# Optimization experiments

Measured on AMD Instinct MI355X. Metric: run time of the kernel, lower is better.

## Reference

```python
import jax, jax.numpy as jnp
import numpy as np

UNITS = 256  # LSTM hidden size per source (units=256)

def setup_inputs() -> dict:
    key = jax.random.key(0)
    ks = jax.random.split(key, 7)
    vocab, embed_dim, seq_len, batch, n_cls = 50000, 256, 512, 64, 20
    x = jax.random.randint(ks[0], (batch, seq_len), 0, vocab)
    emb = jax.random.normal(ks[1], (vocab, embed_dim), jnp.float32) * 0.05
    W = jax.random.normal(ks[2], (embed_dim, 4 * UNITS), jnp.float32) * (1.0 / np.sqrt(embed_dim))
    U = jax.random.normal(ks[3], (UNITS, 4 * UNITS), jnp.float32) * (1.0 / np.sqrt(UNITS))
    # keras unit_forget_bias: forget-gate bias = 1, others 0 (gate order i,f,c,o)
    b = jnp.concatenate([jnp.zeros((UNITS,)), jnp.ones((UNITS,)), jnp.zeros((2 * UNITS,))]).astype(jnp.float32)
    Wd = jax.random.normal(ks[4], (UNITS, n_cls), jnp.float32) * (1.0 / np.sqrt(UNITS))
    bd = jnp.zeros((n_cls,), jnp.float32)
    return {"x": x, "emb": emb, "W": W, "U": U, "b": b, "Wd": Wd, "bd": bd}

def reference(x, emb, W, U, b, Wd, bd):
    # Embedding lookup: [B, T] -> [B, T, D]
    e = emb[x]
    B = e.shape[0]
    # Pre-compute input projections for all timesteps (one big GEMM): [B, T, 4H]
    xz = jnp.einsum('btd,dh->bth', e, W) + b
    h0 = jnp.zeros((B, UNITS), e.dtype)
    c0 = jnp.zeros((B, UNITS), e.dtype)

    def step(carry, zt):
        h, c = carry
        z = zt + h @ U  # [B, 4H]
        i, f, g, o = jnp.split(z, 4, axis=-1)
        i = jax.nn.sigmoid(i)
        f = jax.nn.sigmoid(f)
        g = jnp.tanh(g)
        o = jax.nn.sigmoid(o)
        c_new = f * c + i * g
        h_new = o * jnp.tanh(c_new)
        return (h_new, c_new), None

    (h_T, _), _ = jax.lax.scan(step, (h0, c0), jnp.swapaxes(xz, 0, 1))
    logits = h_T @ Wd + bd
    return jax.nn.softmax(logits, axis=-1)
```

## Files before the change

kernel.cpp:

```cpp
#include <hip/hip_runtime.h>
#include <hip/hip_bf16.h>
#include <math.h>


typedef __bf16 bf16_t;
typedef bf16_t bf16x8 __attribute__((ext_vector_type(8)));
typedef bf16_t bf16x4 __attribute__((ext_vector_type(4)));
typedef float  f32x4  __attribute__((ext_vector_type(4)));

#define T_SZ 512
#define HID 256
#define G4 1024
#define NCLS 20

#define WS_UPACK 0u
#define WS_WPACK (512u * 1024u)
#define WS_HFIN  (1024u * 1024u)
#define WS_EXCH  (1536u * 1024u)
#define WS_XZ    (2u * 1024u * 1024u)

__global__ void pack_weights(const float* __restrict__ W, const float* __restrict__ U,
                             bf16_t* __restrict__ Wp, bf16_t* __restrict__ Up) {
    int tid  = blockIdx.x * blockDim.x + threadIdx.x;
    int j    = tid & 7;
    int lane = (tid >> 3) & 63;
    int ks   = (tid >> 9) & 7;
    int nt   = tid >> 12;
    int row  = ks * 32 + ((lane >> 4) << 3) + j;
    int col  = nt * 16 + (lane & 15);
    Wp[tid] = (bf16_t)W[row * G4 + col];
    Up[tid] = (bf16_t)U[row * G4 + col];
}

__global__ __launch_bounds__(256) void xz_gemm(const int* __restrict__ x,
                                               const float* __restrict__ emb,
                                               const bf16_t* __restrict__ Wp,
                                               const float* __restrict__ bias,
                                               bf16x4* __restrict__ xz2) {
    int nb   = blockIdx.x & 7;
    int t    = blockIdx.x >> 3;
    int w    = threadIdx.x >> 6;
    int lane = threadIdx.x & 63;
    int l15  = lane & 15;
    int quad = lane >> 4;

    int b_row = w * 16 + l15;
    int tok   = x[b_row * T_SZ + t];
    const float* erow = emb + (size_t)tok * 256;

    bf16x8 afrag[8];
#pragma unroll
    for (int ks = 0; ks < 8; ks++) {
        const float4* p = (const float4*)(erow + ks * 32 + quad * 8);
        float4 v0 = p[0], v1 = p[1];
        bf16x8 a;
        a[0] = (bf16_t)v0.x; a[1] = (bf16_t)v0.y; a[2] = (bf16_t)v0.z; a[3] = (bf16_t)v0.w;
        a[4] = (bf16_t)v1.x; a[5] = (bf16_t)v1.y; a[6] = (bf16_t)v1.z; a[7] = (bf16_t)v1.w;
        afrag[ks] = a;
    }

    const bf16x8* Wf = (const bf16x8*)Wp;

#pragma unroll
    for (int nt = 0; nt < 8; nt++) {
        int ntg = nb * 8 + nt;
        float bv = bias[ntg * 16 + l15];
        f32x4 acc = {bv, bv, bv, bv};
        const bf16x8* bp = Wf + (size_t)(ntg * 8) * 64 + lane;
#pragma unroll
        for (int ks = 0; ks < 8; ks++) {
            bf16x8 bfrag = bp[ks * 64];
            acc = __builtin_amdgcn_mfma_f32_16x16x32_bf16(afrag[ks], bfrag, acc, 0, 0, 0);
        }
        bf16x4 hv;
#pragma unroll
        for (int r = 0; r < 4; r++) hv[r] = (bf16_t)acc[r];
        xz2[((size_t)(t * 4 + w) * 64 + ntg) * 64 + lane] = hv;
    }
}

__device__ __forceinline__ float sigmoid_f(float z) {
    return 1.0f / (1.0f + __expf(-z));
}
__device__ __forceinline__ float tanh_f(float z) {
    float e = __expf(2.0f * z);
    return 1.0f - 2.0f / (e + 1.0f);
}
__device__ __forceinline__ unsigned pack2(float a, float b) {
    unsigned short xs = __builtin_bit_cast(unsigned short, (bf16_t)a);
    unsigned short ys = __builtin_bit_cast(unsigned short, (bf16_t)b);
    return (unsigned)xs | ((unsigned)ys << 16);
}
__device__ __forceinline__ bf16_t unpk_lo(unsigned v) {
    return __builtin_bit_cast(bf16_t, (unsigned short)(v & 0xffffu));
}
__device__ __forceinline__ bf16_t unpk_hi(unsigned v) {
    return __builtin_bit_cast(bf16_t, (unsigned short)(v >> 16));
}

__device__ __forceinline__ void mfma_aB(f32x4& d, bf16x8 a, bf16x8 b) {
    asm("v_mfma_f32_16x16x32_bf16 %0, %1, %2, %0" : "+v"(d) : "v"(a), "a"(b));
}

#define POISON 0xAAAAAAAAu

__global__ __launch_bounds__(512, 2) void lstm_pair(const bf16x4* __restrict__ xz2,
                                                    const bf16_t* __restrict__ Up,
                                                    unsigned* __restrict__ exch,
                                                    float* __restrict__ hfin) {
    if (blockIdx.x & 4) return;
    const int g    = blockIdx.x & 3;
    const int p    = (blockIdx.x >> 3) & 1;
    const int w    = threadIdx.x >> 6;
    const int lane = threadIdx.x & 63;
    const int l15  = lane & 15;
    const int quad = lane >> 4;

    __shared__ __align__(16) bf16_t h_lds[2][16][264];

    const bf16x8* Uf = (const bf16x8*)Up + lane;
    bf16x8 u[4][8];
#pragma unroll
    for (int G = 0; G < 4; G++) {
        int ntg = G * 16 + p * 8 + w;
#pragma unroll
        for (int ks = 0; ks < 8; ks++)
            u[G][ks] = Uf[(ntg * 8 + ks) * 64];
    }
    asm volatile("" : "+a"(u[0][0]), "+a"(u[0][1]), "+a"(u[0][2]), "+a"(u[0][3]),
                      "+a"(u[0][4]), "+a"(u[0][5]), "+a"(u[0][6]), "+a"(u[0][7]));
    asm volatile("" : "+a"(u[1][0]), "+a"(u[1][1]), "+a"(u[1][2]), "+a"(u[1][3]),
                      "+a"(u[1][4]), "+a"(u[1][5]), "+a"(u[1][6]), "+a"(u[1][7]));
    asm volatile("" : "+a"(u[2][0]), "+a"(u[2][1]), "+a"(u[2][2]), "+a"(u[2][3]),
                      "+a"(u[2][4]), "+a"(u[2][5]), "+a"(u[2][6]), "+a"(u[2][7]));
    asm volatile("" : "+a"(u[3][0]), "+a"(u[3][1]), "+a"(u[3][2]), "+a"(u[3][3]),
                      "+a"(u[3][4]), "+a"(u[3][5]), "+a"(u[3][6]), "+a"(u[3][7]));

    for (int i = threadIdx.x; i < 2 * 16 * 264; i += 512)
        (&h_lds[0][0][0])[i] = (bf16_t)0.0f;

    f32x4 cst = {0.f, 0.f, 0.f, 0.f};

    bf16x4 xzv[4];
#pragma unroll
    for (int G = 0; G < 4; G++)
        xzv[G] = xz2[((size_t)(0 * 4 + g) * 64 + (G * 16 + p * 8 + w)) * 64 + lane];

    __syncthreads();

    for (int t = 0; t < T_SZ; t++) {
        const int buf  = t & 1;
        const int nbuf = buf ^ 1;

        bf16x8 af[8];
#pragma unroll
        for (int ks = 0; ks < 8; ks++)
            af[ks] = *(const bf16x8*)&h_lds[buf][l15][ks * 32 + quad * 8];

        f32x4 acc[4];
#pragma unroll
        for (int G = 0; G < 4; G++) {
            bf16x4 xv = xzv[G];
            f32x4 a = {(float)xv[0], (float)xv[1], (float)xv[2], (float)xv[3]};
            acc[G] = a;
        }
#pragma unroll
        for (int ks = 0; ks < 8; ks++)
#pragma unroll
            for (int G = 0; G < 4; G++)
                mfma_aB(acc[G], af[ks], u[G][ks]);

        if (t + 1 < T_SZ) {
#pragma unroll
            for (int G = 0; G < 4; G++)
                xzv[G] = xz2[((size_t)((t + 1) * 4 + g) * 64 + (G * 16 + p * 8 + w)) * 64 + lane];
        }

        float hv[4];
#pragma unroll
        for (int r = 0; r < 4; r++) {
            float ig = sigmoid_f(acc[0][r]);
            float fg = sigmoid_f(acc[1][r]);
            float gg = tanh_f(acc[2][r]);
            float og = sigmoid_f(acc[3][r]);
            float cn = fg * cst[r] + ig * gg;
            cst[r] = cn;
            hv[r] = og * tanh_f(cn);
        }

        if (t == T_SZ - 1) {
#pragma unroll
            for (int r = 0; r < 4; r++)
                hfin[(g * 16 + quad * 4 + r) * HID + p * 128 + w * 16 + l15] = hv[r];
            break;
        }

#pragma unroll
        for (int r = 0; r < 4; r++)
            h_lds[nbuf][quad * 4 + r][p * 128 + w * 16 + l15] = (bf16_t)hv[r];

        {
            unsigned dw0 = pack2(hv[0], hv[1]);
            unsigned dw1 = pack2(hv[2], hv[3]);
            unsigned base = (((unsigned)(t & 7) * 4 + (unsigned)g) * 2 + (unsigned)p) * 2048u;
            unsigned di   = (unsigned)(w * 16 + l15) * 8u + (unsigned)(quad * 2);
            __hip_atomic_store(&exch[base + di],          dw0,  __ATOMIC_RELAXED, __HIP_MEMORY_SCOPE_AGENT);
            __hip_atomic_store(&exch[base + di + 1],      dw1,  __ATOMIC_RELAXED, __HIP_MEMORY_SCOPE_AGENT);
            __hip_atomic_store(&exch[base + 1024 + di],     ~dw0, __ATOMIC_RELAXED, __HIP_MEMORY_SCOPE_AGENT);
            __hip_atomic_store(&exch[base + 1024 + di + 1], ~dw1, __ATOMIC_RELAXED, __HIP_MEMORY_SCOPE_AGENT);
        }

        {
            unsigned pbase = (((unsigned)(t & 7) * 4 + (unsigned)g) * 2 + (unsigned)(1 - p)) * 2048u;
            unsigned i0 = (unsigned)threadIdx.x * 2u;
            unsigned d0, d1, m0, m1;
            for (;;) {
                d0 = __hip_atomic_load(&exch[pbase + i0],          __ATOMIC_RELAXED, __HIP_MEMORY_SCOPE_AGENT);
                d1 = __hip_atomic_load(&exch[pbase + i0 + 1],      __ATOMIC_RELAXED, __HIP_MEMORY_SCOPE_AGENT);
                m0 = __hip_atomic_load(&exch[pbase + 1024 + i0],   __ATOMIC_RELAXED, __HIP_MEMORY_SCOPE_AGENT);
                m1 = __hip_atomic_load(&exch[pbase + 1024 + i0 + 1], __ATOMIC_RELAXED, __HIP_MEMORY_SCOPE_AGENT);
                if ((m0 == ~d0) && (m1 == ~d1)) break;
            }
            __hip_atomic_store(&exch[pbase + i0],            POISON, __ATOMIC_RELAXED, __HIP_MEMORY_SCOPE_AGENT);
            __hip_atomic_store(&exch[pbase + i0 + 1],        POISON, __ATOMIC_RELAXED, __HIP_MEMORY_SCOPE_AGENT);
            __hip_atomic_store(&exch[pbase + 1024 + i0],     POISON, __ATOMIC_RELAXED, __HIP_MEMORY_SCOPE_AGENT);
            __hip_atomic_store(&exch[pbase + 1024 + i0 + 1], POISON, __ATOMIC_RELAXED, __HIP_MEMORY_SCOPE_AGENT);
            int lu = (int)(i0 >> 3);
            int qq = (int)((i0 & 7) >> 1);
            int col = (1 - p) * 128 + lu;
            h_lds[nbuf][qq * 4 + 0][col] = unpk_lo(d0);
            h_lds[nbuf][qq * 4 + 1][col] = unpk_hi(d0);
            h_lds[nbuf][qq * 4 + 2][col] = unpk_lo(d1);
            h_lds[nbuf][qq * 4 + 3][col] = unpk_hi(d1);
        }

        __syncthreads();
    }
}

__global__ void head(const float* __restrict__ hfin, const float* __restrict__ Wd,
                     const float* __restrict__ bd, float* __restrict__ out) {
    __shared__ float hrow[HID];
    __shared__ float lg[32];
    __shared__ float ex[32];
    int b = blockIdx.x, tid = threadIdx.x;
    for (int i = tid; i < HID; i += 64) hrow[i] = hfin[b * HID + i];
    __syncthreads();
    if (tid < NCLS) {
        float acc = bd[tid];
        for (int k = 0; k < HID; k++) acc = fmaf(hrow[k], Wd[k * NCLS + tid], acc);
        lg[tid] = acc;
    }
    __syncthreads();
    if (tid < NCLS) {
        float m = -1e30f;
        for (int jj = 0; jj < NCLS; jj++) m = fmaxf(m, lg[jj]);
        ex[tid] = __expf(lg[tid] - m);
    }
    __syncthreads();
    if (tid < NCLS) {
        float sden = 0.0f;
        for (int jj = 0; jj < NCLS; jj++) sden += ex[jj];
        out[b * NCLS + tid] = ex[tid] / sden;
    }
}

extern "C" void kernel_launch(void* const* d_in, const int* in_sizes, int n_in,
                              void* d_out, int out_size, void* d_ws, size_t ws_size,
                              hipStream_t stream) {
    const int*   x    = (const int*)d_in[0];
    const float* emb  = (const float*)d_in[1];
    const float* W    = (const float*)d_in[2];
    const float* U    = (const float*)d_in[3];
    const float* bias = (const float*)d_in[4];
    const float* Wd   = (const float*)d_in[5];
    const float* bd   = (const float*)d_in[6];
    float* out = (float*)d_out;

    char* ws = (char*)d_ws;
    bf16_t*   Up   = (bf16_t*)(ws + WS_UPACK);
    bf16_t*   Wp   = (bf16_t*)(ws + WS_WPACK);
    float*    hf   = (float*)(ws + WS_HFIN);
    unsigned* exch = (unsigned*)(ws + WS_EXCH);
    bf16x4*   xz2  = (bf16x4*)(ws + WS_XZ);

    pack_weights<<<dim3(1024), dim3(256), 0, stream>>>(W, U, Wp, Up);
    xz_gemm<<<dim3(4096), dim3(256), 0, stream>>>(x, emb, Wp, bias, xz2);
    lstm_pair<<<dim3(16), dim3(512), 0, stream>>>(xz2, Up, exch, hf);
    head<<<dim3(64), dim3(64), 0, stream>>>(hf, Wd, bd, out);
}
```

Baseline: 1.721 ms.

## Pack h-exchange payload with epoch-keyed check word into 64-bit atomics

```diff
diff --git a/kernel.cpp b/kernel.cpp
--- a/kernel.cpp
+++ b/kernel.cpp
@@ -7,6 +7,7 @@
 typedef bf16_t bf16x8 __attribute__((ext_vector_type(8)));
 typedef bf16_t bf16x4 __attribute__((ext_vector_type(4)));
 typedef float  f32x4  __attribute__((ext_vector_type(4)));
+typedef unsigned long long u64;
 
 #define T_SZ 512
 #define HID 256
@@ -102,11 +103,9 @@
     asm("v_mfma_f32_16x16x32_bf16 %0, %1, %2, %0" : "+v"(d) : "v"(a), "a"(b));
 }
 
-#define POISON 0xAAAAAAAAu
-
 __global__ __launch_bounds__(512, 2) void lstm_pair(const bf16x4* __restrict__ xz2,
                                                     const bf16_t* __restrict__ Up,
-                                                    unsigned* __restrict__ exch,
+                                                    u64* __restrict__ exch,
                                                     float* __restrict__ hfin) {
     if (blockIdx.x & 4) return;
     const int g    = blockIdx.x & 3;
@@ -151,6 +150,7 @@
     for (int t = 0; t < T_SZ; t++) {
         const int buf  = t & 1;
         const int nbuf = buf ^ 1;
+        const unsigned key = ((unsigned)(t >> 3) + 1u) << 24;
 
         bf16x8 af[8];
 #pragma unroll
@@ -195,39 +195,36 @@
             break;
         }
 
-#pragma unroll
-        for (int r = 0; r < 4; r++)
-            h_lds[nbuf][quad * 4 + r][p * 128 + w * 16 + l15] = (bf16_t)hv[r];
-
         {
             unsigned dw0 = pack2(hv[0], hv[1]);
             unsigned dw1 = pack2(hv[2], hv[3]);
-            unsigned base = (((unsigned)(t & 7) * 4 + (unsigned)g) * 2 + (unsigned)p) * 2048u;
-            unsigned di   = (unsigned)(w * 16 + l15) * 8u + (unsigned)(quad * 2);
-            __hip_atomic_store(&exch[base + di],          dw0,  __ATOMIC_RELAXED, __HIP_MEMORY_SCOPE_AGENT);
-            __hip_atomic_store(&exch[base + di + 1],      dw1,  __ATOMIC_RELAXED, __HIP_MEMORY_SCOPE_AGENT);
-            __hip_atomic_store(&exch[base + 1024 + di],     ~dw0, __ATOMIC_RELAXED, __HIP_MEMORY_SCOPE_AGENT);
-            __hip_atomic_store(&exch[base + 1024 + di + 1], ~dw1, __ATOMIC_RELAXED, __HIP_MEMORY_SCOPE_AGENT);
-        }
+            u64 q0 = (u64)dw0 | ((u64)(dw0 ^ key) << 32);
+            u64 q1 = (u64)dw1 | ((u64)(dw1 ^ key) << 32);
+            unsigned base = (((unsigned)(t & 7) * 4 + (unsigned)g) * 2 + (unsigned)p) * 1024u;
+            unsigned ui   = (unsigned)(w * 16 + l15) * 8u + (unsigned)(quad * 2);
+            __hip_atomic_store(&exch[base + ui],     q0, __ATOMIC_RELAXED, __HIP_MEMORY_SCOPE_AGENT);
+            __hip_atomic_store(&exch[base + ui + 1], q1, __ATOMIC_RELAXED, __HIP_MEMORY_SCOPE_AGENT);
+        }
+
+#pragma unroll
+        for (int r = 0; r < 4; r++)
+            h_lds[nbuf][quad * 4 + r][p * 128 + w * 16 + l15] = (bf16_t)hv[r];
 
         {
-            unsigned pbase = (((unsigned)(t & 7) * 4 + (unsigned)g) * 2 + (unsigned)(1 - p)) * 2048u;
+            unsigned pbase = (((unsigned)(t & 7) * 4 + (unsigned)g) * 2 + (unsigned)(1 - p)) * 1024u;
             unsigned i0 = (unsigned)threadIdx.x * 2u;
-            unsigned d0, d1, m0, m1;
+            u64 q0, q1;
             for (;;) {
-                d0 = __hip_atomic_load(&exch[pbase + i0],          __ATOMIC_RELAXED, __HIP_MEMORY_SCOPE_AGENT);
-                d1 = __hip_atomic_load(&exch[pbase + i0 + 1],      __ATOMIC_RELAXED, __HIP_MEMORY_SCOPE_AGENT);
-                m0 = __hip_atomic_load(&exch[pbase + 1024 + i0],   __ATOMIC_RELAXED, __HIP_MEMORY_SCOPE_AGENT);
-                m1 = __hip_atomic_load(&exch[pbase + 1024 + i0 + 1], __ATOMIC_RELAXED, __HIP_MEMORY_SCOPE_AGENT);
-                if ((m0 == ~d0) && (m1 == ~d1)) break;
+                q0 = __hip_atomic_load(&exch[pbase + i0],     __ATOMIC_RELAXED, __HIP_MEMORY_SCOPE_AGENT);
+                q1 = __hip_atomic_load(&exch[pbase + i0 + 1], __ATOMIC_RELAXED, __HIP_MEMORY_SCOPE_AGENT);
+                bool v0 = ((unsigned)(q0 >> 32)) == (((unsigned)q0) ^ key);
+                bool v1 = ((unsigned)(q1 >> 32)) == (((unsigned)q1) ^ key);
+                if (v0 && v1) break;
             }
-            __hip_atomic_store(&exch[pbase + i0],            POISON, __ATOMIC_RELAXED, __HIP_MEMORY_SCOPE_AGENT);
-            __hip_atomic_store(&exch[pbase + i0 + 1],        POISON, __ATOMIC_RELAXED, __HIP_MEMORY_SCOPE_AGENT);
-            __hip_atomic_store(&exch[pbase + 1024 + i0],     POISON, __ATOMIC_RELAXED, __HIP_MEMORY_SCOPE_AGENT);
-            __hip_atomic_store(&exch[pbase + 1024 + i0 + 1], POISON, __ATOMIC_RELAXED, __HIP_MEMORY_SCOPE_AGENT);
-            int lu = (int)(i0 >> 3);
-            int qq = (int)((i0 & 7) >> 1);
-            int col = (1 - p) * 128 + lu;
+            unsigned d0 = (unsigned)q0, d1 = (unsigned)q1;
+            int ul  = (int)(i0 >> 3);
+            int qq  = (int)((i0 & 7) >> 1);
+            int col = (1 - p) * 128 + ul;
             h_lds[nbuf][qq * 4 + 0][col] = unpk_lo(d0);
             h_lds[nbuf][qq * 4 + 1][col] = unpk_hi(d0);
             h_lds[nbuf][qq * 4 + 2][col] = unpk_lo(d1);
@@ -278,11 +275,11 @@
     float* out = (float*)d_out;
 
     char* ws = (char*)d_ws;
-    bf16_t*   Up   = (bf16_t*)(ws + WS_UPACK);
-    bf16_t*   Wp   = (bf16_t*)(ws + WS_WPACK);
-    float*    hf   = (float*)(ws + WS_HFIN);
-    unsigned* exch = (unsigned*)(ws + WS_EXCH);
-    bf16x4*   xz2  = (bf16x4*)(ws + WS_XZ);
+    bf16_t* Up   = (bf16_t*)(ws + WS_UPACK);
+    bf16_t* Wp   = (bf16_t*)(ws + WS_WPACK);
+    float*  hf   = (float*)(ws + WS_HFIN);
+    u64*    exch = (u64*)(ws + WS_EXCH);
+    bf16x4* xz2  = (bf16x4*)(ws + WS_XZ);
 
     pack_weights<<<dim3(1024), dim3(256), 0, stream>>>(W, U, Wp, Up);
     xz_gemm<<<dim3(4096), dim3(256), 0, stream>>>(x, emb, Wp, bias, xz2);
```

Result: faster. 1.458 ms (-15.3%).
